# Performance work log

Measured on AMD Instinct MI355X. Metric: run time of the kernel, lower is better.

The kernel has to match this reference:

```python
import jax, jax.numpy as jnp
import numpy as np

B, N, H, L, K, R = 1024, 64, 128, 4, 16, 20
CUTOFF = 5.0
GAMMA = 10.0   # RBF width
N_TYPES = 10

def _rn(k, shape, scale):
    return jax.random.normal(k, shape, jnp.float32) * scale

def setup_inputs():
    key = jax.random.key(0)
    ks = jax.random.split(key, 16)
    z = lambda *s: jnp.zeros(s, jnp.float32)
    return {
        "positions": _rn(ks[0], (B, N, 3), 2.0),
        "atomic_numbers": jax.random.randint(ks[1], (B, N), 0, N_TYPES),
        "atom_embed": _rn(ks[2], (N_TYPES, H // 4), 0.1),
        "pos_W": _rn(ks[3], (3, 3 * H // 4), 0.5),
        "pos_b": z(3 * H // 4),
        "msg_W": _rn(ks[4], (L, 2 * H + R, H), (2 * H + R) ** -0.5),
        "msg_b": z(L, H),
        "upd_W": _rn(ks[5], (L, H, H), H ** -0.5),
        "upd_b": z(L, H),
        "gself_W": _rn(ks[6], (L, H, H), H ** -0.5),
        "gmean_W": _rn(ks[7], (L, H, H), H ** -0.5),
        "g_b": z(L, H),
        "fus_W": _rn(ks[8], (L, 2 * H, H), (2 * H) ** -0.5),
        "fus_b": z(L, H),
        "ln_g": jnp.ones((L, H), jnp.float32),
        "ln_b": z(L, H),
        "cb_W1": _rn(ks[9], (L, H, 4 * H), H ** -0.5),
        "cb_b1": z(L, 4 * H),
        "cb_W2": _rn(ks[10], (L, 4 * H, H), (4 * H) ** -0.5),
        "cb_b2": z(L, H),
        "fo_W1": _rn(ks[11], (H, H), H ** -0.5),
        "fo_b1": z(H),
        "fo_W2": _rn(ks[12], (H, 3), H ** -0.5),
        "fo_b2": z(3),
    }

def _ln(x, g, b):
    m = x.mean(-1, keepdims=True)
    v = ((x - m) ** 2).mean(-1, keepdims=True)
    return (x - m) * jax.lax.rsqrt(v + 1e-5) * g + b

def reference(positions, atomic_numbers, atom_embed, pos_W, pos_b, msg_W, msg_b,
              upd_W, upd_b, gself_W, gmean_W, g_b, fus_W, fus_b, ln_g, ln_b,
              cb_W1, cb_b1, cb_W2, cb_b2, fo_W1, fo_b1, fo_W2, fo_b2):
    silu = jax.nn.silu
    Bb, Nn, _ = positions.shape
    # embeddings: atom type (H/4) || position (3H/4)
    h = jnp.concatenate([atom_embed[atomic_numbers], positions @ pos_W + pos_b], -1)  # [B,N,H]
    # kNN graph from positions (static across layers since positions are fixed)
    diff = positions[:, :, None, :] - positions[:, None, :, :]
    d2 = jnp.sum(diff * diff, -1) + jnp.eye(Nn, dtype=positions.dtype) * 1e9  # exclude self
    neg_d2, idx = jax.lax.top_k(-d2, K)                       # [B,N,K]
    d = jnp.sqrt(jnp.maximum(-neg_d2, 1e-12))
    centers = jnp.linspace(0.0, CUTOFF, R).astype(positions.dtype)
    rbf = jnp.exp(-GAMMA * (d[..., None] - centers) ** 2)     # [B,N,K,R]
    env = (0.5 * (jnp.cos(jnp.pi * d / CUTOFF) + 1.0) * (d < CUTOFF))[..., None]  # cosine cutoff
    idx_flat = idx.reshape(Bb, Nn * K)
    for i in range(msg_W.shape[0]):
        # local MPNN: gather neighbors, message MLP on [h_i, h_j, rbf], envelope, sum
        h_j = jnp.take_along_axis(h, idx_flat[:, :, None], axis=1).reshape(Bb, Nn, K, -1)
        h_i = jnp.broadcast_to(h[:, :, None, :], h_j.shape)
        m = silu(jnp.concatenate([h_i, h_j, rbf], -1) @ msg_W[i] + msg_b[i]) * env
        local = h + silu(m.sum(2) @ upd_W[i] + upd_b[i])
        # Clifford mean-field: self transform + global-mean transform
        glob = silu(h @ gself_W[i] + h.mean(1, keepdims=True) @ gmean_W[i] + g_b[i])
        # fusion (dropout is identity at inference)
        fused = silu(jnp.concatenate([local, glob], -1) @ fus_W[i] + fus_b[i])
        # Clifford block: pre-LN residual MLP
        x = _ln(fused, ln_g[i], ln_b[i])
        h = fused + silu(x @ cb_W1[i] + cb_b1[i]) @ cb_W2[i] + cb_b2[i]
    return silu(h @ fo_W1 + fo_b1) @ fo_W2 + fo_b2  # [B,N,3] forces
```

## Files before the change

kernel.cpp:

```cpp
#include <hip/hip_runtime.h>

typedef unsigned short ushort_t;
typedef unsigned int uint_t;
typedef unsigned long long ull_t;
typedef __attribute__((ext_vector_type(8))) short short8;
typedef __attribute__((ext_vector_type(4))) float f32x4;

#define B_ 1024
#define N_ 64
#define H_ 128
#define NT 256

#define IMG_WI 0
#define IMG_WJ 16384
#define IMG_UW 32768
#define IMG_GS 49152
#define IMG_FT 65536
#define IMG_FB 81920
#define IMG_C1 98304
#define IMG_C2 163840
#define IMG_GMT 229376
#define IMG_RW 245760
#define IMG_L 249856
#define IMG_FO 999424

__device__ __forceinline__ ushort_t f2bf(float f) {
    return __builtin_bit_cast(ushort_t, (__bf16)f);
}
__device__ __forceinline__ float bf2f(ushort_t u) {
    union { uint_t i; float f; } v; v.i = ((uint_t)u) << 16; return v.f;
}
__device__ __forceinline__ float siluf(float x) { return x / (1.0f + __expf(-x)); }

__device__ __forceinline__ int sidx(int m, int k) {
    return m * H_ + (((k >> 3) ^ (m & 7)) << 3) + (k & 7);
}
__device__ __forceinline__ int fragoff(int m, int ch) {
    return m * H_ + ((ch ^ (m & 7)) << 3);
}

extern "C" __global__ __launch_bounds__(256)
void convert_weights(const float* __restrict__ msg_W, const float* __restrict__ upd_W,
                     const float* __restrict__ gself_W, const float* __restrict__ fus_W,
                     const float* __restrict__ cb_W1, const float* __restrict__ cb_W2,
                     const float* __restrict__ gmean_W, const float* __restrict__ fo_W1,
                     ushort_t* __restrict__ wimg)
{
    __shared__ ushort_t tile[128][34];
    const int g = blockIdx.x;
    const int tid = threadIdx.x;
    const float* W; int ld = 128, k0 = 0, c0; ushort_t* dst;
    if (g >= 244) {
        int st = g - 244;
        W = fo_W1; c0 = st * 32; dst = wimg + IMG_FO + st * 4096;
    } else {
        const int l = g / 61, r = g - l * 61;
        ushort_t* base = wimg + l * IMG_L;
        if (r == 60) {
            const float* Wr = msg_W + l * 35328 + 256 * 128;
            ushort_t* drw = base + IMG_RW;
            for (int e = 0; e < 16; ++e) {
                int q = threadIdx.x * 16 + e;
                int sub = q >> 10, n = (q >> 5) & 31, k = q & 31;
                drw[q] = f2bf(k < 20 ? Wr[(size_t)k * 128 + sub * 32 + n] : 0.0f);
            }
            return;
        }
        int off, st;
        if      (r < 4)  { W = msg_W + l * 35328;            st = r;      off = IMG_WI;  c0 = st * 32; }
        else if (r < 8)  { W = msg_W + l * 35328;  k0 = 128; st = r - 4;  off = IMG_WJ;  c0 = st * 32; }
        else if (r < 12) { W = upd_W + l * 16384;            st = r - 8;  off = IMG_UW;  c0 = st * 32; }
        else if (r < 16) { W = gself_W + l * 16384;          st = r - 12; off = IMG_GS;  c0 = st * 32; }
        else if (r < 20) { W = fus_W + l * 32768;            st = r - 16; off = IMG_FT;  c0 = st * 32; }
        else if (r < 24) { W = fus_W + l * 32768;  k0 = 128; st = r - 20; off = IMG_FB;  c0 = st * 32; }
        else if (r < 40) { W = cb_W1 + l * 65536;  ld = 512; st = r - 24; off = IMG_C1;  c0 = st * 32; }
        else if (r < 56) { int j = (r - 40) >> 2; W = cb_W2 + l * 65536; k0 = j * 128;
                           st = r - 40; off = IMG_C2; c0 = ((r - 40) & 3) * 32; }
        else             { W = gmean_W + l * 16384;          st = r - 56; off = IMG_GMT; c0 = st * 32; }
        dst = base + off + st * 4096;
    }
    const int kr = tid >> 5, n = tid & 31;
    #pragma unroll
    for (int p = 0; p < 16; ++p) {
        int k = p * 8 + kr;
        tile[k][n] = f2bf(W[(size_t)(k0 + k) * ld + c0 + n]);
    }
    __syncthreads();
    {
        int n2 = tid >> 3, kk = (tid & 7) << 4;
        short8 v0, v1;
        #pragma unroll
        for (int e = 0; e < 8; ++e) v0[e] = (short)tile[kk + e][n2];
        #pragma unroll
        for (int e = 0; e < 8; ++e) v1[e] = (short)tile[kk + 8 + e][n2];
        *(short8*)(dst + n2 * 128 + kk) = v0;
        *(short8*)(dst + n2 * 128 + kk + 8) = v1;
    }
}

struct __align__(16) Smem {
    ushort_t T1[N_ * H_];
    ushort_t T2[N_ * H_];
    ushort_t T3[N_ * H_];
    float d[1024];
    float env[1024];
    ushort_t idx[1024];
    char u[2048];
};

__device__ __forceinline__ f32x4 gemm_s(const short8 a[4], const ushort_t* __restrict__ img,
                                        int s, int l15, int quad)
{
    const ushort_t* base = img + ((s >> 1) << 12) + ((((s & 1) << 4) + l15) << 7) + quad * 8;
    short8 b0 = *(const short8*)(base);
    short8 b1 = *(const short8*)(base + 32);
    short8 b2 = *(const short8*)(base + 64);
    short8 b3 = *(const short8*)(base + 96);
    f32x4 c = {0.f, 0.f, 0.f, 0.f};
    c = __builtin_amdgcn_mfma_f32_16x16x32_bf16(a[0], b0, c, 0, 0, 0);
    c = __builtin_amdgcn_mfma_f32_16x16x32_bf16(a[1], b1, c, 0, 0, 0);
    c = __builtin_amdgcn_mfma_f32_16x16x32_bf16(a[2], b2, c, 0, 0, 0);
    c = __builtin_amdgcn_mfma_f32_16x16x32_bf16(a[3], b3, c, 0, 0, 0);
    return c;
}
__device__ __forceinline__ f32x4 gemm_s_acc(const short8 a[4], const ushort_t* __restrict__ img,
                                            int s, int l15, int quad, f32x4 c)
{
    const ushort_t* base = img + ((s >> 1) << 12) + ((((s & 1) << 4) + l15) << 7) + quad * 8;
    short8 b0 = *(const short8*)(base);
    short8 b1 = *(const short8*)(base + 32);
    short8 b2 = *(const short8*)(base + 64);
    short8 b3 = *(const short8*)(base + 96);
    c = __builtin_amdgcn_mfma_f32_16x16x32_bf16(a[0], b0, c, 0, 0, 0);
    c = __builtin_amdgcn_mfma_f32_16x16x32_bf16(a[1], b1, c, 0, 0, 0);
    c = __builtin_amdgcn_mfma_f32_16x16x32_bf16(a[2], b2, c, 0, 0, 0);
    c = __builtin_amdgcn_mfma_f32_16x16x32_bf16(a[3], b3, c, 0, 0, 0);
    return c;
}
__device__ __forceinline__ void loadA(const ushort_t* __restrict__ X, int mrow, int quad, short8 a[4]) {
    #pragma unroll
    for (int kc = 0; kc < 4; ++kc) a[kc] = *(const short8*)&X[fragoff(mrow, kc * 4 + quad)];
}

extern "C" __global__ __launch_bounds__(NT, 2)
void md17_fused_kernel(
    const float* __restrict__ positions, const int* __restrict__ atomic_numbers,
    const float* __restrict__ atom_embed, const float* __restrict__ pos_W,
    const float* __restrict__ pos_b,
    const float* __restrict__ msg_b, const float* __restrict__ upd_b,
    const float* __restrict__ g_b, const float* __restrict__ fus_b,
    const float* __restrict__ ln_g, const float* __restrict__ ln_b,
    const float* __restrict__ cb_b1, const float* __restrict__ cb_b2,
    const float* __restrict__ fo_b1,
    const float* __restrict__ fo_W2, const float* __restrict__ fo_b2,
    char* __restrict__ ws, float* __restrict__ out)
{
    __shared__ Smem sm;
    const int b = blockIdx.x;
    const int tid = threadIdx.x;
    const int wave = tid >> 6, lane = tid & 63;
    const int quad = lane >> 4, l15 = lane & 15;
    const int mrow = wave * 16 + l15;
    const int rbase = wave * 16 + quad * 4;

    const ushort_t* wimg = (const ushort_t*)ws;
    float* spos = (float*)sm.u;
    ushort_t* part = (ushort_t*)sm.u;
    float* hmean = (float*)(sm.u + 1024);
    float* gvec  = (float*)(sm.u + 1536);

    float hreg[8][4];

    {
        float px = positions[b * 192 + lane * 3 + 0];
        float py = positions[b * 192 + lane * 3 + 1];
        float pz = positions[b * 192 + lane * 3 + 2];
        if (tid < 192) spos[tid] = positions[b * 192 + tid];
        #pragma unroll 1
        for (int g = 0; g < 16; ++g) {
            int n = wave * 16 + g;
            float dx = __fsub_rn(__shfl(px, n), px);
            float dy = __fsub_rn(__shfl(py, n), py);
            float dz = __fsub_rn(__shfl(pz, n), pz);
            float d2 = __fadd_rn(__fadd_rn(__fmul_rn(dx, dx), __fmul_rn(dy, dy)), __fmul_rn(dz, dz));
            if (lane == n) d2 = 1e30f;
            float sd = 0.f; int si = 0;
            for (int k = 0; k < 16; ++k) {
                float dmin = d2;
                #pragma unroll
                for (int o = 1; o < 64; o <<= 1) dmin = fminf(dmin, __shfl_xor(dmin, o));
                ull_t mask = __ballot(d2 == dmin);
                int widx = __ffsll(mask) - 1;
                if (lane == widx) d2 = 1e30f;
                if (lane == k) { si = widx; sd = dmin; }
            }
            if (lane < 16) {
                float dd = sqrtf(fmaxf(sd, 1e-12f));
                sm.d[n * 16 + lane] = dd;
                sm.env[n * 16 + lane] = (dd < 5.0f) ? 0.5f * (__cosf(0.62831853071795864769f * dd) + 1.0f) : 0.0f;
                sm.idx[n * 16 + lane] = (ushort_t)si;
            }
        }
    }
    __syncthreads();
    {
        int an[4];
        #pragma unroll
        for (int r = 0; r < 4; ++r) an[r] = atomic_numbers[b * N_ + rbase + r];
        #pragma unroll
        for (int s = 0; s < 8; ++s) {
            int col = s * 16 + l15;
            #pragma unroll
            for (int r = 0; r < 4; ++r) {
                float v;
                if (s < 2) {
                    v = atom_embed[an[r] * 32 + col];
                } else {
                    int j = col - 32;
                    v = pos_b[j];
                    #pragma unroll
                    for (int c = 0; c < 3; ++c)
                        v = fmaf(spos[(rbase + r) * 3 + c], pos_W[c * 96 + j], v);
                }
                hreg[s][r] = v;
                sm.T3[sidx(rbase + r, col)] = f2bf(v);
            }
        }
    }
    __syncthreads();
    #pragma unroll
    for (int s = 0; s < 8; ++s) {
        int col = s * 16 + l15;
        float p = hreg[s][0] + hreg[s][1] + hreg[s][2] + hreg[s][3];
        p += __shfl_xor(p, 16);
        p += __shfl_xor(p, 32);
        if (quad == 0) part[wave * 128 + col] = f2bf(p);
    }

    #pragma unroll 1
    for (int l = 0; l < 4; ++l) {
        const ushort_t* wl = wimg + l * IMG_L;
        const float* mb  = msg_b + l * H_;
        const float* ub  = upd_b + l * H_;
        const float* gb  = g_b + l * H_;
        const float* fb  = fus_b + l * H_;
        const float* lg  = ln_g + l * H_;
        const float* lb  = ln_b + l * H_;
        const float* c1b = cb_b1 + l * 4 * H_;
        const float* c2b = cb_b2 + l * H_;

        __syncthreads();
        if (tid < H_)
            hmean[tid] = (bf2f(part[tid]) + bf2f(part[128 + tid])
                        + bf2f(part[256 + tid]) + bf2f(part[384 + tid])) * (1.0f / 64.0f);
        __syncthreads();

        if (tid < H_) {
            float s = gb[tid];
            const ushort_t* wrow = wl + IMG_GMT + tid * 128;
            for (int c = 0; c < 128; c += 8) {
                short8 w = *(const short8*)(wrow + c);
                #pragma unroll
                for (int i = 0; i < 8; ++i) s = fmaf(hmean[c + i], bf2f((ushort_t)w[i]), s);
            }
            gvec[tid] = s;
        }
        {
            short8 a_h[4]; loadA(sm.T3, mrow, quad, a_h);
            #pragma unroll
            for (int s = 0; s < 8; ++s) {
                f32x4 c = gemm_s(a_h, wl + IMG_WI, s, l15, quad);
                int col = s * 16 + l15; float bv = mb[col];
                #pragma unroll
                for (int r = 0; r < 4; ++r)
                    sm.T1[sidx(rbase + r, col)] = f2bf(c[r] + bv);
            }
            #pragma unroll
            for (int s = 0; s < 8; ++s) {
                f32x4 c = gemm_s(a_h, wl + IMG_WJ, s, l15, quad);
                int col = s * 16 + l15;
                #pragma unroll
                for (int r = 0; r < 4; ++r)
                    sm.T2[sidx(rbase + r, col)] = f2bf(c[r]);
            }
        }
        __syncthreads();

        {
            float ccv[8];
            #pragma unroll
            for (int j = 0; j < 8; ++j)
                ccv[j] = (float)((double)(quad * 8 + j) * (5.0 / 19.0));
            short8 brw[8];
            #pragma unroll
            for (int s = 0; s < 8; ++s)
                brw[s] = *(const short8*)(wl + IMG_RW + ((s >> 1) << 10)
                                          + ((((s & 1) << 4) + l15) << 5) + quad * 8);
            #pragma unroll 1
            for (int g = 0; g < 16; ++g) {
                int n = wave * 16 + g;
                int jv[4]; float ev[4];
                #pragma unroll
                for (int r = 0; r < 4; ++r) {
                    int k = quad * 4 + r;
                    jv[r] = sm.idx[n * 16 + k];
                    ev[r] = sm.env[n * 16 + k];
                }
                float ddm = sm.d[n * 16 + l15];
                short8 arb;
                #pragma unroll
                for (int j = 0; j < 8; ++j) {
                    float t2 = ddm - ccv[j];
                    float rv = __expf(-10.0f * t2 * t2);
                    arb[j] = (short)((quad * 8 + j) < 20 ? f2bf(rv) : (ushort_t)0);
                }
                #pragma unroll
                for (int s = 0; s < 8; ++s) {
                    int col = s * 16 + l15;
                    f32x4 c = {0.f, 0.f, 0.f, 0.f};
                    c = __builtin_amdgcn_mfma_f32_16x16x32_bf16(arb, brw[s], c, 0, 0, 0);
                    float ai = bf2f(sm.T1[sidx(n, col)]);
                    float acc = 0.f;
                    #pragma unroll
                    for (int r = 0; r < 4; ++r) {
                        float gm = bf2f(sm.T2[sidx(jv[r], col)]);
                        acc = fmaf(siluf(ai + gm + c[r]), ev[r], acc);
                    }
                    acc += __shfl_xor(acc, 16);
                    acc += __shfl_xor(acc, 32);
                    if (quad == 0) sm.T1[sidx(n, col)] = f2bf(acc);
                }
            }
        }
        __syncthreads();


        {
            short8 a_m[4]; loadA(sm.T1, mrow, quad, a_m);
            #pragma unroll
            for (int s = 0; s < 8; ++s) {
                f32x4 c = gemm_s(a_m, wl + IMG_UW, s, l15, quad);
                int col = s * 16 + l15; float bv = ub[col];
                #pragma unroll
                for (int r = 0; r < 4; ++r)
                    sm.T2[sidx(rbase + r, col)] = f2bf(hreg[s][r] + siluf(c[r] + bv));
            }
            short8 a_h[4]; loadA(sm.T3, mrow, quad, a_h);
            #pragma unroll
            for (int s = 0; s < 8; ++s) {
                f32x4 c = gemm_s(a_h, wl + IMG_GS, s, l15, quad);
                int col = s * 16 + l15; float gv = gvec[col];
                #pragma unroll
                for (int r = 0; r < 4; ++r)
                    sm.T1[sidx(rbase + r, col)] = f2bf(siluf(c[r] + gv));
            }
        }

        float sr[4] = {0.f, 0.f, 0.f, 0.f}, qr[4] = {0.f, 0.f, 0.f, 0.f};
        {
            short8 a_t[4];
            loadA(sm.T2, mrow, quad, a_t);
            #pragma unroll
            for (int s = 0; s < 8; ++s) {
                f32x4 c = gemm_s(a_t, wl + IMG_FT, s, l15, quad);
                #pragma unroll
                for (int r = 0; r < 4; ++r) hreg[s][r] = c[r];
            }
            loadA(sm.T1, mrow, quad, a_t);
            #pragma unroll
            for (int s = 0; s < 8; ++s) {
                f32x4 c = gemm_s(a_t, wl + IMG_FB, s, l15, quad);
                int col = s * 16 + l15; float bv = fb[col];
                #pragma unroll
                for (int r = 0; r < 4; ++r) {
                    float v = siluf(hreg[s][r] + c[r] + bv);
                    hreg[s][r] = v;
                    sr[r] += v; qr[r] += v * v;
                }
            }
            #pragma unroll
            for (int o = 1; o < 16; o <<= 1) {
                #pragma unroll
                for (int r = 0; r < 4; ++r) {
                    sr[r] += __shfl_xor(sr[r], o);
                    qr[r] += __shfl_xor(qr[r], o);
                }
            }
        }

        #pragma unroll
        for (int r = 0; r < 4; ++r) {
            float mu = sr[r] * (1.0f / 128.0f);
            float var = qr[r] * (1.0f / 128.0f) - mu * mu;
            float rs = rsqrtf(var + 1e-5f);
            int row = rbase + r;
            #pragma unroll
            for (int s = 0; s < 8; ++s) {
                int col = s * 16 + l15;
                sm.T1[sidx(row, col)] = f2bf((hreg[s][r] - mu) * rs * lg[col] + lb[col]);
            }
        }

        {
            f32x4 acc2[8];
            #pragma unroll
            for (int s = 0; s < 8; ++s) {
                int col = s * 16 + l15; float bv = c2b[col];
                #pragma unroll
                for (int r = 0; r < 4; ++r) acc2[s][r] = hreg[s][r] + bv;
            }
            #pragma unroll 1
            for (int j = 0; j < 4; ++j) {
                short8 a_x[4]; loadA(sm.T1, mrow, quad, a_x);
                #pragma unroll
                for (int s = 0; s < 8; ++s) {
                    f32x4 c = gemm_s(a_x, wl + IMG_C1 + j * 16384, s, l15, quad);
                    int col = s * 16 + l15; float bv = c1b[j * H_ + col];
                    #pragma unroll
                    for (int r = 0; r < 4; ++r)
                        sm.T2[sidx(rbase + r, col)] = f2bf(siluf(c[r] + bv));
                }
                short8 a_t[4]; loadA(sm.T2, mrow, quad, a_t);
                #pragma unroll
                for (int s = 0; s < 8; ++s)
                    acc2[s] = gemm_s_acc(a_t, wl + IMG_C2 + j * 16384, s, l15, quad, acc2[s]);
            }
            #pragma unroll
            for (int s = 0; s < 8; ++s) {
                int col = s * 16 + l15;
                float p = 0.f;
                #pragma unroll
                for (int r = 0; r < 4; ++r) {
                    float v = acc2[s][r];
                    hreg[s][r] = v;
                    sm.T3[sidx(rbase + r, col)] = f2bf(v);
                    p += v;
                }
                p += __shfl_xor(p, 16);
                p += __shfl_xor(p, 32);
                if (quad == 0) part[wave * 128 + col] = f2bf(p);
            }
        }
    }

    {
        short8 a_f[4]; loadA(sm.T3, mrow, quad, a_f);
        #pragma unroll
        for (int s = 0; s < 8; ++s) {
            f32x4 c = gemm_s(a_f, wimg + IMG_FO, s, l15, quad);
            int col = s * 16 + l15; float bv = fo_b1[col];
            #pragma unroll
            for (int r = 0; r < 4; ++r)
                sm.T2[sidx(rbase + r, col)] = f2bf(siluf(c[r] + bv));
        }
    }
    __syncthreads();
    if (tid < 192) {
        int n = tid / 3, j = tid - n * 3;
        float s = fo_b2[j];
        #pragma unroll 1
        for (int ch = 0; ch < 16; ++ch) {
            short8 v = *(const short8*)&sm.T2[fragoff(n, ch)];
            #pragma unroll
            for (int i = 0; i < 8; ++i)
                s = fmaf(bf2f((ushort_t)v[i]), fo_W2[(ch * 8 + i) * 3 + j], s);
        }
        out[b * 192 + tid] = s;
    }
}

extern "C" void kernel_launch(void* const* d_in, const int* in_sizes, int n_in,
                              void* d_out, int out_size, void* d_ws, size_t ws_size,
                              hipStream_t stream) {
    (void)in_sizes; (void)n_in; (void)out_size; (void)ws_size;
    convert_weights<<<248, 256, 0, stream>>>(
        (const float*)d_in[5], (const float*)d_in[7], (const float*)d_in[9],
        (const float*)d_in[12], (const float*)d_in[16], (const float*)d_in[18],
        (const float*)d_in[10], (const float*)d_in[20], (ushort_t*)d_ws);
    md17_fused_kernel<<<B_, NT, 0, stream>>>(
        (const float*)d_in[0], (const int*)d_in[1],
        (const float*)d_in[2], (const float*)d_in[3], (const float*)d_in[4],
        (const float*)d_in[6], (const float*)d_in[8],
        (const float*)d_in[11], (const float*)d_in[13],
        (const float*)d_in[14], (const float*)d_in[15],
        (const float*)d_in[17], (const float*)d_in[19],
        (const float*)d_in[21],
        (const float*)d_in[22], (const float*)d_in[23],
        (char*)d_ws, (float*)d_out);
}
```

Baseline: 1.347 ms.

## Parallelize kNN across 16-lane groups and cut register pressure in GEMM loops

The kNN top-k selection is rewritten so each wave handles four atoms at once. Each 16-lane group scans four candidates per lane, which takes fewer shuffle steps per selection and a quarter of the outer iterations. The RBF weight fragments are now loaded inside the message loop instead of being held in eight registers. Several GEMM column loops drop from full unroll to unroll 2. Both register changes aim to lower VGPR use and possibly raise occupancy, at the cost of reloading weights from memory and less instruction-level parallelism.

```diff
diff --git a/kernel.cpp b/kernel.cpp
--- a/kernel.cpp
+++ b/kernel.cpp
@@ -171,38 +171,59 @@
 
     float hreg[8][4];
 
+    if (tid < 192) spos[tid] = positions[b * 192 + tid];
+    __syncthreads();
+
     {
-        float px = positions[b * 192 + lane * 3 + 0];
-        float py = positions[b * 192 + lane * 3 + 1];
-        float pz = positions[b * 192 + lane * 3 + 2];
-        if (tid < 192) spos[tid] = positions[b * 192 + tid];
+        float cx[4], cy[4], cz[4];
+        #pragma unroll
+        for (int j = 0; j < 4; ++j) {
+            cx[j] = spos[(l15 * 4 + j) * 3 + 0];
+            cy[j] = spos[(l15 * 4 + j) * 3 + 1];
+            cz[j] = spos[(l15 * 4 + j) * 3 + 2];
+        }
         #pragma unroll 1
-        for (int g = 0; g < 16; ++g) {
-            int n = wave * 16 + g;
-            float dx = __fsub_rn(__shfl(px, n), px);
-            float dy = __fsub_rn(__shfl(py, n), py);
-            float dz = __fsub_rn(__shfl(pz, n), pz);
-            float d2 = __fadd_rn(__fadd_rn(__fmul_rn(dx, dx), __fmul_rn(dy, dy)), __fmul_rn(dz, dz));
-            if (lane == n) d2 = 1e30f;
-            float sd = 0.f; int si = 0;
+        for (int it = 0; it < 4; ++it) {
+            const int n = wave * 16 + it * 4 + quad;
+            float nx = spos[n * 3 + 0], ny = spos[n * 3 + 1], nz = spos[n * 3 + 2];
+            float d2[4];
+            #pragma unroll
+            for (int j = 0; j < 4; ++j) {
+                float dx = __fsub_rn(nx, cx[j]);
+                float dy = __fsub_rn(ny, cy[j]);
+                float dz = __fsub_rn(nz, cz[j]);
+                d2[j] = __fadd_rn(__fadd_rn(__fmul_rn(dx, dx), __fmul_rn(dy, dy)),
+                                  __fmul_rn(dz, dz));
+                if (l15 * 4 + j == n) d2[j] = 1e30f;
+            }
+            #pragma unroll 1
             for (int k = 0; k < 16; ++k) {
-                float dmin = d2;
-                #pragma unroll
-                for (int o = 1; o < 64; o <<= 1) dmin = fminf(dmin, __shfl_xor(dmin, o));
-                ull_t mask = __ballot(d2 == dmin);
-                int widx = __ffsll(mask) - 1;
-                if (lane == widx) d2 = 1e30f;
-                if (lane == k) { si = widx; sd = dmin; }
-            }
-            if (lane < 16) {
-                float dd = sqrtf(fmaxf(sd, 1e-12f));
-                sm.d[n * 16 + lane] = dd;
-                sm.env[n * 16 + lane] = (dd < 5.0f) ? 0.5f * (__cosf(0.62831853071795864769f * dd) + 1.0f) : 0.0f;
-                sm.idx[n * 16 + lane] = (ushort_t)si;
-            }
-        }
-    }
-    __syncthreads();
+                float lm = d2[0];
+                if (d2[1] < lm) lm = d2[1];
+                if (d2[2] < lm) lm = d2[2];
+                if (d2[3] < lm) lm = d2[3];
+                float gm = lm;
+                #pragma unroll
+                for (int o = 1; o < 16; o <<= 1) gm = fminf(gm, __shfl_xor(gm, o));
+                ull_t bal = __ballot(lm == gm);
+                int wl = __ffsll((bal >> (quad * 16)) & 0xFFFFull) - 1;
+                if (l15 == wl) {
+                    int jstar = 3;
+                    if (d2[2] == gm) jstar = 2;
+                    if (d2[1] == gm) jstar = 1;
+                    if (d2[0] == gm) jstar = 0;
+                    #pragma unroll
+                    for (int j = 0; j < 4; ++j) if (j == jstar) d2[j] = 1e30f;
+                    float dd = sqrtf(fmaxf(gm, 1e-12f));
+                    sm.d[n * 16 + k] = dd;
+                    sm.env[n * 16 + k] = (dd < 5.0f)
+                        ? 0.5f * (__cosf(0.62831853071795864769f * dd) + 1.0f) : 0.0f;
+                    sm.idx[n * 16 + k] = (ushort_t)(wl * 4 + jstar);
+                }
+            }
+        }
+    }
+
     {
         int an[4];
         #pragma unroll
@@ -267,7 +288,7 @@
         }
         {
             short8 a_h[4]; loadA(sm.T3, mrow, quad, a_h);
-            #pragma unroll
+            #pragma unroll 2
             for (int s = 0; s < 8; ++s) {
                 f32x4 c = gemm_s(a_h, wl + IMG_WI, s, l15, quad);
                 int col = s * 16 + l15; float bv = mb[col];
@@ -275,7 +296,7 @@
                 for (int r = 0; r < 4; ++r)
                     sm.T1[sidx(rbase + r, col)] = f2bf(c[r] + bv);
             }
-            #pragma unroll
+            #pragma unroll 2
             for (int s = 0; s < 8; ++s) {
                 f32x4 c = gemm_s(a_h, wl + IMG_WJ, s, l15, quad);
                 int col = s * 16 + l15;
@@ -291,11 +312,6 @@
             #pragma unroll
             for (int j = 0; j < 8; ++j)
                 ccv[j] = (float)((double)(quad * 8 + j) * (5.0 / 19.0));
-            short8 brw[8];
-            #pragma unroll
-            for (int s = 0; s < 8; ++s)
-                brw[s] = *(const short8*)(wl + IMG_RW + ((s >> 1) << 10)
-                                          + ((((s & 1) << 4) + l15) << 5) + quad * 8);
             #pragma unroll 1
             for (int g = 0; g < 16; ++g) {
                 int n = wave * 16 + g;
@@ -317,8 +333,11 @@
                 #pragma unroll
                 for (int s = 0; s < 8; ++s) {
                     int col = s * 16 + l15;
+                    const ushort_t* rbase_p = wl + IMG_RW + ((s >> 1) << 10)
+                                            + ((((s & 1) << 4) + l15) << 5) + quad * 8;
+                    short8 brw = *(const short8*)rbase_p;
                     f32x4 c = {0.f, 0.f, 0.f, 0.f};
-                    c = __builtin_amdgcn_mfma_f32_16x16x32_bf16(arb, brw[s], c, 0, 0, 0);
+                    c = __builtin_amdgcn_mfma_f32_16x16x32_bf16(arb, brw, c, 0, 0, 0);
                     float ai = bf2f(sm.T1[sidx(n, col)]);
                     float acc = 0.f;
                     #pragma unroll
@@ -346,7 +365,7 @@
                     sm.T2[sidx(rbase + r, col)] = f2bf(hreg[s][r] + siluf(c[r] + bv));
             }
             short8 a_h[4]; loadA(sm.T3, mrow, quad, a_h);
-            #pragma unroll
+            #pragma unroll 2
             for (int s = 0; s < 8; ++s) {
                 f32x4 c = gemm_s(a_h, wl + IMG_GS, s, l15, quad);
                 int col = s * 16 + l15; float gv = gvec[col];
@@ -412,7 +431,7 @@
             #pragma unroll 1
             for (int j = 0; j < 4; ++j) {
                 short8 a_x[4]; loadA(sm.T1, mrow, quad, a_x);
-                #pragma unroll
+                #pragma unroll 2
                 for (int s = 0; s < 8; ++s) {
                     f32x4 c = gemm_s(a_x, wl + IMG_C1 + j * 16384, s, l15, quad);
                     int col = s * 16 + l15; float bv = c1b[j * H_ + col];
@@ -445,7 +464,7 @@
 
     {
         short8 a_f[4]; loadA(sm.T3, mrow, quad, a_f);
-        #pragma unroll
+        #pragma unroll 2
         for (int s = 0; s < 8; ++s) {
             f32x4 c = gemm_s(a_f, wimg + IMG_FO, s, l15, quad);
             int col = s * 16 + l15; float bv = fo_b1[col];
```

Result: faster. 1.204 ms, median of 2 (-10.6%).
